# Optimization experiments

Measured on AMD Instinct MI355X. Metric: run time of the kernel, lower is better.

The kernel has to match this reference:

```python
import jax, jax.numpy as jnp
import numpy as np

RULE_START = 85
N_RULE = 20
N_OUTPUT = 33
N_RNN = 1024
T, B = 256, 256
ALPHA = 0.2
SIGMA = 0.05


def setup_inputs() -> dict:
    key = jax.random.key(0)
    ks = jax.random.split(key, 9)
    x = jax.random.normal(ks[0], (T, B, RULE_START + N_RULE), dtype=jnp.float32)
    # torch.rand_like -> uniform [0,1), scaled by sigma_rec (precomputed for all steps)
    noise = jax.random.uniform(ks[1], (T, B, N_RNN), dtype=jnp.float32) * SIGMA
    s = 0.05  # small init scale to keep softplus in a sane range
    W_sens = jax.random.normal(ks[2], (N_RNN, RULE_START), dtype=jnp.float32) * s
    b_sens = jax.random.normal(ks[3], (N_RNN,), dtype=jnp.float32) * s
    W_rule = jax.random.normal(ks[4], (N_RNN, N_RULE), dtype=jnp.float32) * s
    W_rec = jax.random.normal(ks[5], (N_RNN, N_RNN), dtype=jnp.float32) * s
    b_rec = jax.random.normal(ks[6], (N_RNN,), dtype=jnp.float32) * s
    W_out = jax.random.normal(ks[7], (N_OUTPUT, N_RNN), dtype=jnp.float32) * s
    b_out = jax.random.normal(ks[8], (N_OUTPUT,), dtype=jnp.float32) * s
    return {"x": x, "noise": noise, "W_sens": W_sens, "b_sens": b_sens,
            "W_rule": W_rule, "W_rec": W_rec, "b_rec": b_rec,
            "W_out": W_out, "b_out": b_out}


def reference(x, noise, W_sens, b_sens, W_rule, W_rec, b_rec, W_out, b_out):
    # x: [T, B, rule_start + n_rule]
    sensory = x[:, :, :RULE_START]
    rule = x[:, :, RULE_START:]
    # input projections applied once for all timesteps: [T, B, H]
    rnn_inputs = (jnp.einsum('tbi,hi->tbh', sensory, W_sens) + b_sens
                  + jnp.einsum('tbr,hr->tbh', rule, W_rule))

    h0 = jnp.zeros_like(rnn_inputs[0])  # [B, H]

    def step(h, inp_nz):
        inp, nz = inp_nz
        out = jax.nn.softplus(inp + nz + h @ W_rec.T + b_rec)
        h = ALPHA * out + (1.0 - ALPHA) * h
        return h, h

    _, hidden_states = jax.lax.scan(step, h0, (rnn_inputs, noise))  # [T, B, H]
    return jnp.einsum('tbh,oh->tbo', hidden_states, W_out) + b_out
```

## Files before the change

### kernel.cpp

```cpp
#include <hip/hip_runtime.h>
#include <cstdint>
#include <cstddef>

#define TSTEPS 256
#define NB     256
#define NH     1024
#define NIN    105
#define NOUT   33

using half8 = __attribute__((ext_vector_type(8))) _Float16;
using f32x4 = __attribute__((ext_vector_type(4))) float;


__global__ __launch_bounds__(256) void k_convert(
    const float* __restrict__ W_sens, const float* __restrict__ W_rule,
    const float* __restrict__ W_rec,  const float* __restrict__ W_out,
    _Float16* __restrict__ Wrecf, _Float16* __restrict__ Wcf,
    _Float16* __restrict__ Wof)
{
    int tid  = blockIdx.x * 256 + threadIdx.x;
    int lane = tid & 63;
    int orow = lane & 15;
    int col0 = (lane >> 4) * 8;
    if (tid < 64 * 32 * 64) {
        int kk = (tid >> 6) & 31, n = tid >> 11;
        int o = n * 16 + orow, k0 = kk * 32 + col0;
        const float* s = W_rec + (size_t)o * NH + k0;
        _Float16* d = Wrecf + (size_t)tid * 8;
        #pragma unroll
        for (int j = 0; j < 8; ++j) d[j] = (_Float16)s[j];
    } else if (tid < 64 * 32 * 64 + 64 * 4 * 64) {
        int t2 = tid - 64 * 32 * 64;
        int kk = (t2 >> 6) & 3, n = t2 >> 8;
        int o = n * 16 + orow, k0 = kk * 32 + col0;
        _Float16* d = Wcf + (size_t)t2 * 8;
        #pragma unroll
        for (int j = 0; j < 8; ++j) {
            int k = k0 + j;
            float v = 0.f;
            if (k < 85)       v = W_sens[o * 85 + k];
            else if (k < NIN) v = W_rule[o * 20 + (k - 85)];
            d[j] = (_Float16)v;
        }
    } else {
        int t3 = tid - (64 * 32 * 64 + 64 * 4 * 64);
        int kk = (t3 >> 6) & 31, n = t3 >> 11;
        int o = n * 16 + orow, k0 = kk * 32 + col0;
        _Float16* d = Wof + (size_t)t3 * 8;
        #pragma unroll
        for (int j = 0; j < 8; ++j)
            d[j] = (o < NOUT) ? (_Float16)W_out[(size_t)o * NH + k0 + j]
                              : (_Float16)0.f;
    }
}

__global__ __launch_bounds__(256) void k_init(int* __restrict__ flags)
{
    if (threadIdx.x < 256) flags[threadIdx.x] = 0;
}

__device__ __forceinline__ void in_gemm(
    const float* __restrict__ x, int tstep, int g, int m, int mrow, int q,
    const half8 wcb[4][4], const float nzf[4][4], const float bias[4],
    f32x4 pA[4])
{
    const float* xrow = x + ((size_t)tstep * NB + g * 32 + m * 16 + mrow) * NIN;
    half8 af[4];
    #pragma unroll
    for (int kk = 0; kk < 4; ++kk) {
        #pragma unroll
        for (int j = 0; j < 8; ++j) {
            int c = kk * 32 + q * 8 + j;
            float v = (c < NIN) ? xrow[c] : 0.f;
            af[kk][j] = (_Float16)v;
        }
    }
    #pragma unroll
    for (int nt = 0; nt < 4; ++nt) {
        f32x4 c = { nzf[nt][0] + bias[nt], nzf[nt][1] + bias[nt],
                    nzf[nt][2] + bias[nt], nzf[nt][3] + bias[nt] };
        #pragma unroll
        for (int kk = 0; kk < 4; ++kk)
            c = __builtin_amdgcn_mfma_f32_16x16x32_f16(af[kk], wcb[nt][kk], c,
                                                       0, 0, 0);
        pA[nt] = c;
    }
}

__global__ __launch_bounds__(512, 1) void k_rnn(
    const float* __restrict__ x, float* __restrict__ noise,
    const float* __restrict__ b_sens, const float* __restrict__ b_rec,
    const _Float16* __restrict__ Wrecf, const _Float16* __restrict__ Wcf,
    int* __restrict__ arr, int* __restrict__ xcdArr)
{
    __shared__ _Float16 Wl[4 * 32 * 64 * 8];
    __shared__ float red[3][8][64][4];
    __shared__ int sFast;

    const int tid  = threadIdx.x;
    const int blk  = blockIdx.x;
    const int g    = blk & 7, s = blk >> 3;
    const int wave = tid >> 6, lane = tid & 63;
    const int m    = wave & 1, kq = wave >> 1;
    const int mrow = lane & 15, q = lane >> 4;
    const half8* Wc8 = (const half8*)Wcf;
    _Float16* hist = (_Float16*)noise;
    volatile int* varr = (volatile int*)arr;

    {
        const float4* src = (const float4*)(Wrecf + (size_t)(4 * s) * (32 * 64 * 8));
        float4* dst = (float4*)Wl;
        for (int i = tid; i < 8192; i += 512) dst[i] = src[i];
    }

    int xcd;
    asm volatile("s_getreg_b32 %0, hwreg(20, 0, 4)" : "=s"(xcd));
    if (tid == 0)
        __hip_atomic_store(&xcdArr[blk], xcd + 1, __ATOMIC_RELEASE,
                           __HIP_MEMORY_SCOPE_AGENT);
    if (wave == 0) {
        int idx = g + (lane & 15) * 8;
        int v = 0;
        for (int it = 0; it < (1 << 22); ++it) {
            v = __hip_atomic_load(&xcdArr[idx], __ATOMIC_ACQUIRE,
                                  __HIP_MEMORY_SCOPE_AGENT);
            if (__all(v >= 1)) break;
            __builtin_amdgcn_s_sleep(8);
        }
        if (lane == 0) sFast = __all(v == xcd + 1) ? 1 : 0;
    }
    __syncthreads();
    const bool fast = (sFast != 0);

    float hm[4][4];
    f32x4 pA[4];
    float nzf[4][4];
    float bias[4];
    half8 wcb[4][4];
    #pragma unroll
    for (int nt = 0; nt < 4; ++nt)
        #pragma unroll
        for (int r = 0; r < 4; ++r) hm[nt][r] = 0.f;

    if (kq == 0) {
        #pragma unroll
        for (int nt = 0; nt < 4; ++nt) {
            int o = s * 64 + nt * 16 + mrow;
            bias[nt] = b_sens[o] + b_rec[o];
            #pragma unroll
            for (int kk = 0; kk < 4; ++kk)
                wcb[nt][kk] = Wc8[((4 * s + nt) * 4 + kk) * 64 + lane];
            #pragma unroll
            for (int r = 0; r < 4; ++r)
                nzf[nt][r] = noise[(size_t)(g * 32 + m * 16 + q * 4 + r) * NH
                                   + s * 64 + nt * 16 + mrow];
        }
    }
    __syncthreads();
    if (tid == 0) {
        if (fast) varr[g * 16 + s] = 1;
        else __hip_atomic_store(&arr[g * 16 + s], 1, __ATOMIC_RELAXED,
                                __HIP_MEMORY_SCOPE_AGENT);
    }
    if (kq == 0)
        in_gemm(x, 0, g, m, mrow, q, wcb, nzf, bias, pA);

    for (int t = 0; t < TSTEPS; ++t) {
        if (kq == 0 && t + 1 < TSTEPS) {
            #pragma unroll
            for (int nt = 0; nt < 4; ++nt)
                #pragma unroll
                for (int r = 0; r < 4; ++r)
                    nzf[nt][r] = noise[((size_t)(t + 1) * NB + g * 32 + m * 16
                                        + q * 4 + r) * NH
                                       + s * 64 + nt * 16 + mrow];
        }
        if (wave == 0) {
            int idx = g * 16 + (lane & 15);
            if (fast) {
                for (int it = 0; it < (1 << 22); ++it) {
                    asm volatile("buffer_inv sc0" ::: "memory");
                    int v = varr[idx];
                    if (__all(v >= t + 1)) break;
                    __builtin_amdgcn_s_sleep(1);
                }
            } else {
                for (int it = 0; it < (1 << 22); ++it) {
                    int v = __hip_atomic_load(&arr[idx], __ATOMIC_RELAXED,
                                              __HIP_MEMORY_SCOPE_AGENT);
                    if (__all(v >= t + 1)) break;
                    __builtin_amdgcn_s_sleep(1);
                }
            }
        }
        asm volatile("s_barrier" ::: "memory");
        if (!fast) __builtin_amdgcn_fence(__ATOMIC_ACQUIRE, "agent");

        f32x4 acc[4];
        #pragma unroll
        for (int nt = 0; nt < 4; ++nt) acc[nt] = (f32x4){0.f, 0.f, 0.f, 0.f};
        if (t > 0) {
            const _Float16* hR = hist + (size_t)(t - 1) * 524288
                                      + (size_t)g * 65536
                                      + (size_t)(m * 16 + mrow) * 1024
                                      + kq * 256 + q * 8;
            #pragma unroll
            for (int kkl = 0; kkl < 8; ++kkl) {
                half8 a = *(const half8*)(hR + kkl * 32);
                #pragma unroll
                for (int nt = 0; nt < 4; ++nt) {
                    half8 b = *(const half8*)&Wl[((nt * 32 + kq * 8 + kkl) * 64
                                                  + lane) * 8];
                    acc[nt] = __builtin_amdgcn_mfma_f32_16x16x32_f16(a, b,
                                                                acc[nt], 0, 0, 0);
                }
            }
        }
        if (kq != 0) {
            #pragma unroll
            for (int nt = 0; nt < 4; ++nt)
                *(f32x4*)&red[kq - 1][m * 4 + nt][lane][0] = acc[nt];
        }
        asm volatile("s_waitcnt lgkmcnt(0)\n\ts_barrier" ::: "memory");

        if (kq == 0) {
            const size_t hb = (size_t)t * 524288 + (size_t)g * 65536;
            #pragma unroll
            for (int nt = 0; nt < 4; ++nt) {
                f32x4 r0 = *(const f32x4*)&red[0][m * 4 + nt][lane][0];
                f32x4 r1 = *(const f32x4*)&red[1][m * 4 + nt][lane][0];
                f32x4 r2 = *(const f32x4*)&red[2][m * 4 + nt][lane][0];
                #pragma unroll
                for (int r = 0; r < 4; ++r) {
                    float v  = acc[nt][r] + r0[r] + r1[r] + r2[r] + pA[nt][r];
                    float sp = fmaxf(v, 0.f) + __logf(1.f + __expf(-fabsf(v)));
                    float hn = 0.2f * sp + 0.8f * hm[nt][r];
                    hm[nt][r] = hn;
                    hist[hb + (size_t)(m * 16 + q * 4 + r) * 1024
                            + s * 64 + nt * 16 + mrow] = (_Float16)hn;
                }
            }
        }
        asm volatile("s_waitcnt vmcnt(0) lgkmcnt(0)\n\ts_barrier" ::: "memory");
        if (tid == 0) {
            if (fast) varr[g * 16 + s] = t + 2;
            else {
                __builtin_amdgcn_fence(__ATOMIC_RELEASE, "agent");
                __hip_atomic_store(&arr[g * 16 + s], t + 2, __ATOMIC_RELAXED,
                                   __HIP_MEMORY_SCOPE_AGENT);
            }
        }
        if (kq == 0 && t + 1 < TSTEPS)
            in_gemm(x, t + 1, g, m, mrow, q, wcb, nzf, bias, pA);
    }
}

__global__ __launch_bounds__(256) void k_out(
    const _Float16* __restrict__ h16, const _Float16* __restrict__ Wof,
    const float* __restrict__ b_out, float* __restrict__ y)
{
    int blk  = blockIdx.x;
    int wave = threadIdx.x >> 6, lane = threadIdx.x & 63;
    int mrow = lane & 15, q = lane >> 4;
    int t  = blk >> 2;
    int b  = (blk & 3) * 64 + wave * 16 + mrow;
    size_t hb = (size_t)t * 524288 + (size_t)(b >> 5) * 65536
              + (size_t)(b & 31) * 1024;
    const half8* Wo8 = (const half8*)Wof;

    f32x4 acc[3];
    #pragma unroll
    for (int nt = 0; nt < 3; ++nt) acc[nt] = (f32x4){0.f, 0.f, 0.f, 0.f};

    #pragma unroll 4
    for (int kk = 0; kk < 32; ++kk) {
        half8 a = *(const half8*)(h16 + hb + kk * 32 + q * 8);
        #pragma unroll
        for (int nt = 0; nt < 3; ++nt) {
            half8 bb = Wo8[(nt * 32 + kk) * 64 + lane];
            acc[nt] = __builtin_amdgcn_mfma_f32_16x16x32_f16(a, bb, acc[nt],
                                                             0, 0, 0);
        }
    }
    #pragma unroll
    for (int nt = 0; nt < 3; ++nt) {
        int o = nt * 16 + mrow;
        if (o < NOUT) {
            float bo = b_out[o];
            #pragma unroll
            for (int r = 0; r < 4; ++r) {
                size_t R = (size_t)blk * 64 + wave * 16 + q * 4 + r;
                y[R * NOUT + o] = acc[nt][r] + bo;
            }
        }
    }
}

extern "C" void kernel_launch(void* const* d_in, const int* in_sizes, int n_in,
                              void* d_out, int out_size, void* d_ws, size_t ws_size,
                              hipStream_t stream) {
    const float* x      = (const float*)d_in[0];
    float*       noise  = (float*)d_in[1];
    const float* W_sens = (const float*)d_in[2];
    const float* b_sens = (const float*)d_in[3];
    const float* W_rule = (const float*)d_in[4];
    const float* W_rec  = (const float*)d_in[5];
    const float* b_rec  = (const float*)d_in[6];
    const float* W_out  = (const float*)d_in[7];
    const float* b_out  = (const float*)d_in[8];
    float*       y      = (float*)d_out;

    _Float16* wsp   = (_Float16*)d_ws;
    _Float16* Wrecf = wsp;
    _Float16* Wcf   = Wrecf + 1048576;
    _Float16* Wof   = Wcf   + 131072;
    int*      arr   = (int*)(Wof + 49152);
    int*      xcdArr= arr + 128;

    k_convert<<<dim3(600), dim3(256), 0, stream>>>(W_sens, W_rule, W_rec, W_out,
                                                   Wrecf, Wcf, Wof);
    k_init<<<dim3(1), dim3(256), 0, stream>>>(arr);
    k_rnn<<<dim3(128), dim3(512), 0, stream>>>(x, noise, b_sens, b_rec,
                                               Wrecf, Wcf, arr, xcdArr);
    k_out<<<dim3(1024), dim3(256), 0, stream>>>((const _Float16*)noise, Wof,
                                                b_out, y);
}
```

Baseline: 1.698 ms.

## Keep W_rec slice in registers and offload input projection to a dedicated wave

The recurrent kernel moves from 8 waves with W_rec staged in LDS to 6 waves. Four compute waves each hold their K-slice of W_rec in registers and process both 16-row M tiles. A fifth wave computes the next step's input projection plus noise into a double-buffered LDS array, and a sixth wave polls the inter-block flags. The cross-wave reduction now spreads the softplus/update work over all four compute waves instead of one K-quarter. The aim is to take the input GEMM off the serial critical path and remove LDS reads of the weights, at the cost of much higher register pressure (32 half8 weight registers per lane).

```diff
diff --git a/kernel.cpp b/kernel.cpp
--- a/kernel.cpp
+++ b/kernel.cpp
@@ -59,59 +59,25 @@
     if (threadIdx.x < 256) flags[threadIdx.x] = 0;
 }
 
-__device__ __forceinline__ void in_gemm(
-    const float* __restrict__ x, int tstep, int g, int m, int mrow, int q,
-    const half8 wcb[4][4], const float nzf[4][4], const float bias[4],
-    f32x4 pA[4])
-{
-    const float* xrow = x + ((size_t)tstep * NB + g * 32 + m * 16 + mrow) * NIN;
-    half8 af[4];
-    #pragma unroll
-    for (int kk = 0; kk < 4; ++kk) {
-        #pragma unroll
-        for (int j = 0; j < 8; ++j) {
-            int c = kk * 32 + q * 8 + j;
-            float v = (c < NIN) ? xrow[c] : 0.f;
-            af[kk][j] = (_Float16)v;
-        }
-    }
-    #pragma unroll
-    for (int nt = 0; nt < 4; ++nt) {
-        f32x4 c = { nzf[nt][0] + bias[nt], nzf[nt][1] + bias[nt],
-                    nzf[nt][2] + bias[nt], nzf[nt][3] + bias[nt] };
-        #pragma unroll
-        for (int kk = 0; kk < 4; ++kk)
-            c = __builtin_amdgcn_mfma_f32_16x16x32_f16(af[kk], wcb[nt][kk], c,
-                                                       0, 0, 0);
-        pA[nt] = c;
-    }
-}
-
-__global__ __launch_bounds__(512, 1) void k_rnn(
+__global__ __launch_bounds__(384, 2) void k_rnn(
     const float* __restrict__ x, float* __restrict__ noise,
     const float* __restrict__ b_sens, const float* __restrict__ b_rec,
     const _Float16* __restrict__ Wrecf, const _Float16* __restrict__ Wcf,
     int* __restrict__ arr, int* __restrict__ xcdArr)
 {
-    __shared__ _Float16 Wl[4 * 32 * 64 * 8];
-    __shared__ float red[3][8][64][4];
+    __shared__ float red[4][2][3][64][4];
+    __shared__ float pAl[2][2][4][64][4];
     __shared__ int sFast;
 
     const int tid  = threadIdx.x;
     const int blk  = blockIdx.x;
     const int g    = blk & 7, s = blk >> 3;
     const int wave = tid >> 6, lane = tid & 63;
-    const int m    = wave & 1, kq = wave >> 1;
     const int mrow = lane & 15, q = lane >> 4;
+    const half8* Wr8 = (const half8*)Wrecf;
     const half8* Wc8 = (const half8*)Wcf;
     _Float16* hist = (_Float16*)noise;
     volatile int* varr = (volatile int*)arr;
-
-    {
-        const float4* src = (const float4*)(Wrecf + (size_t)(4 * s) * (32 * 64 * 8));
-        float4* dst = (float4*)Wl;
-        for (int i = tid; i < 8192; i += 512) dst[i] = src[i];
-    }
 
     int xcd;
     asm volatile("s_getreg_b32 %0, hwreg(20, 0, 4)" : "=s"(xcd));
@@ -129,53 +95,91 @@
         }
         if (lane == 0) sFast = __all(v == xcd + 1) ? 1 : 0;
     }
+
+    half8 bf[4][8];
+    float hm[2][4];
+    half8 wcb[4][4];
+    float bias4[4];
+
+    if (wave < 4) {
+        #pragma unroll
+        for (int nt = 0; nt < 4; ++nt)
+            #pragma unroll
+            for (int kkl = 0; kkl < 8; ++kkl)
+                bf[nt][kkl] =
+                    Wr8[(size_t)((4 * s + nt) * 32 + wave * 8 + kkl) * 64 + lane];
+        #pragma unroll
+        for (int m = 0; m < 2; ++m)
+            #pragma unroll
+            for (int r = 0; r < 4; ++r) hm[m][r] = 0.f;
+    } else if (wave == 4) {
+        #pragma unroll
+        for (int nt = 0; nt < 4; ++nt) {
+            int o = s * 64 + nt * 16 + mrow;
+            bias4[nt] = b_sens[o] + b_rec[o];
+            #pragma unroll
+            for (int kk = 0; kk < 4; ++kk)
+                wcb[nt][kk] = Wc8[((4 * s + nt) * 4 + kk) * 64 + lane];
+        }
+        #pragma unroll
+        for (int m = 0; m < 2; ++m) {
+            const float* xrow = x + (size_t)(g * 32 + m * 16 + mrow) * NIN;
+            half8 af[4];
+            #pragma unroll
+            for (int kk = 0; kk < 4; ++kk)
+                #pragma unroll
+                for (int j = 0; j < 8; ++j) {
+                    int c = kk * 32 + q * 8 + j;
+                    af[kk][j] = (_Float16)((c < NIN) ? xrow[c] : 0.f);
+                }
+            #pragma unroll
+            for (int nt = 0; nt < 4; ++nt) {
+                f32x4 c;
+                #pragma unroll
+                for (int r = 0; r < 4; ++r)
+                    c[r] = noise[(size_t)(g * 32 + m * 16 + q * 4 + r) * NH
+                                 + s * 64 + nt * 16 + mrow] + bias4[nt];
+                #pragma unroll
+                for (int kk = 0; kk < 4; ++kk)
+                    c = __builtin_amdgcn_mfma_f32_16x16x32_f16(af[kk],
+                                                        wcb[nt][kk], c, 0, 0, 0);
+                *(f32x4*)&pAl[0][m][nt][lane][0] = c;
+            }
+        }
+    }
     __syncthreads();
     const bool fast = (sFast != 0);
-
-    float hm[4][4];
-    f32x4 pA[4];
-    float nzf[4][4];
-    float bias[4];
-    half8 wcb[4][4];
-    #pragma unroll
-    for (int nt = 0; nt < 4; ++nt)
-        #pragma unroll
-        for (int r = 0; r < 4; ++r) hm[nt][r] = 0.f;
-
-    if (kq == 0) {
-        #pragma unroll
-        for (int nt = 0; nt < 4; ++nt) {
-            int o = s * 64 + nt * 16 + mrow;
-            bias[nt] = b_sens[o] + b_rec[o];
-            #pragma unroll
-            for (int kk = 0; kk < 4; ++kk)
-                wcb[nt][kk] = Wc8[((4 * s + nt) * 4 + kk) * 64 + lane];
-            #pragma unroll
-            for (int r = 0; r < 4; ++r)
-                nzf[nt][r] = noise[(size_t)(g * 32 + m * 16 + q * 4 + r) * NH
-                                   + s * 64 + nt * 16 + mrow];
-        }
-    }
-    __syncthreads();
     if (tid == 0) {
         if (fast) varr[g * 16 + s] = 1;
         else __hip_atomic_store(&arr[g * 16 + s], 1, __ATOMIC_RELAXED,
                                 __HIP_MEMORY_SCOPE_AGENT);
     }
-    if (kq == 0)
-        in_gemm(x, 0, g, m, mrow, q, wcb, nzf, bias, pA);
 
     for (int t = 0; t < TSTEPS; ++t) {
-        if (kq == 0 && t + 1 < TSTEPS) {
-            #pragma unroll
-            for (int nt = 0; nt < 4; ++nt)
-                #pragma unroll
-                for (int r = 0; r < 4; ++r)
-                    nzf[nt][r] = noise[((size_t)(t + 1) * NB + g * 32 + m * 16
-                                        + q * 4 + r) * NH
-                                       + s * 64 + nt * 16 + mrow];
-        }
-        if (wave == 0) {
+        float xf[2][4][8];
+        float nzv[2][4][4];
+        if (wave == 4 && t + 1 < TSTEPS) {
+            #pragma unroll
+            for (int m = 0; m < 2; ++m) {
+                const float* xrow = x + ((size_t)(t + 1) * NB + g * 32 + m * 16
+                                         + mrow) * NIN;
+                #pragma unroll
+                for (int kk = 0; kk < 4; ++kk)
+                    #pragma unroll
+                    for (int j = 0; j < 8; ++j) {
+                        int c = kk * 32 + q * 8 + j;
+                        xf[m][kk][j] = (c < NIN) ? xrow[c] : 0.f;
+                    }
+                #pragma unroll
+                for (int nt = 0; nt < 4; ++nt)
+                    #pragma unroll
+                    for (int r = 0; r < 4; ++r)
+                        nzv[m][nt][r] =
+                            noise[((size_t)(t + 1) * NB + g * 32 + m * 16
+                                   + q * 4 + r) * NH + s * 64 + nt * 16 + mrow];
+            }
+        }
+        if (wave == 5) {
             int idx = g * 16 + (lane & 15);
             if (fast) {
                 for (int it = 0; it < (1 << 22); ++it) {
@@ -196,48 +200,88 @@
         asm volatile("s_barrier" ::: "memory");
         if (!fast) __builtin_amdgcn_fence(__ATOMIC_ACQUIRE, "agent");
 
-        f32x4 acc[4];
-        #pragma unroll
-        for (int nt = 0; nt < 4; ++nt) acc[nt] = (f32x4){0.f, 0.f, 0.f, 0.f};
-        if (t > 0) {
+        f32x4 acc[2][4];
+        #pragma unroll
+        for (int m = 0; m < 2; ++m)
+            #pragma unroll
+            for (int nt = 0; nt < 4; ++nt) acc[m][nt] = (f32x4){0.f,0.f,0.f,0.f};
+        if (wave < 4 && t > 0) {
             const _Float16* hR = hist + (size_t)(t - 1) * 524288
-                                      + (size_t)g * 65536
-                                      + (size_t)(m * 16 + mrow) * 1024
-                                      + kq * 256 + q * 8;
+                                      + (size_t)g * 65536 + wave * 256 + q * 8;
             #pragma unroll
             for (int kkl = 0; kkl < 8; ++kkl) {
-                half8 a = *(const half8*)(hR + kkl * 32);
+                half8 a0 = *(const half8*)(hR + (size_t)mrow * 1024 + kkl * 32);
+                half8 a1 = *(const half8*)(hR + (size_t)(16 + mrow) * 1024
+                                              + kkl * 32);
                 #pragma unroll
                 for (int nt = 0; nt < 4; ++nt) {
-                    half8 b = *(const half8*)&Wl[((nt * 32 + kq * 8 + kkl) * 64
-                                                  + lane) * 8];
-                    acc[nt] = __builtin_amdgcn_mfma_f32_16x16x32_f16(a, b,
-                                                                acc[nt], 0, 0, 0);
-                }
-            }
-        }
-        if (kq != 0) {
-            #pragma unroll
-            for (int nt = 0; nt < 4; ++nt)
-                *(f32x4*)&red[kq - 1][m * 4 + nt][lane][0] = acc[nt];
+                    acc[0][nt] = __builtin_amdgcn_mfma_f32_16x16x32_f16(
+                                     a0, bf[nt][kkl], acc[0][nt], 0, 0, 0);
+                    acc[1][nt] = __builtin_amdgcn_mfma_f32_16x16x32_f16(
+                                     a1, bf[nt][kkl], acc[1][nt], 0, 0, 0);
+                }
+            }
+        }
+        if (wave == 4 && t + 1 < TSTEPS) {
+            const int buf = (t + 1) & 1;
+            #pragma unroll
+            for (int m = 0; m < 2; ++m) {
+                half8 af[4];
+                #pragma unroll
+                for (int kk = 0; kk < 4; ++kk)
+                    #pragma unroll
+                    for (int j = 0; j < 8; ++j)
+                        af[kk][j] = (_Float16)xf[m][kk][j];
+                #pragma unroll
+                for (int nt = 0; nt < 4; ++nt) {
+                    f32x4 c = { nzv[m][nt][0] + bias4[nt],
+                                nzv[m][nt][1] + bias4[nt],
+                                nzv[m][nt][2] + bias4[nt],
+                                nzv[m][nt][3] + bias4[nt] };
+                    #pragma unroll
+                    for (int kk = 0; kk < 4; ++kk)
+                        c = __builtin_amdgcn_mfma_f32_16x16x32_f16(
+                                af[kk], wcb[nt][kk], c, 0, 0, 0);
+                    *(f32x4*)&pAl[buf][m][nt][lane][0] = c;
+                }
+            }
+        }
+        if (wave < 4) {
+            #pragma unroll
+            for (int m = 0; m < 2; ++m)
+                #pragma unroll
+                for (int nt = 0; nt < 4; ++nt)
+                    if (nt != wave) {
+                        int slot = (wave < nt) ? wave : wave - 1;
+                        *(f32x4*)&red[nt][m][slot][lane][0] = acc[m][nt];
+                    }
         }
         asm volatile("s_waitcnt lgkmcnt(0)\n\ts_barrier" ::: "memory");
 
-        if (kq == 0) {
+        if (wave < 4) {
+            f32x4 own[2];
+            #pragma unroll
+            for (int m = 0; m < 2; ++m) {
+                own[m] = acc[m][0];
+                #pragma unroll
+                for (int nt = 1; nt < 4; ++nt)
+                    if (wave == nt) own[m] = acc[m][nt];
+            }
             const size_t hb = (size_t)t * 524288 + (size_t)g * 65536;
             #pragma unroll
-            for (int nt = 0; nt < 4; ++nt) {
-                f32x4 r0 = *(const f32x4*)&red[0][m * 4 + nt][lane][0];
-                f32x4 r1 = *(const f32x4*)&red[1][m * 4 + nt][lane][0];
-                f32x4 r2 = *(const f32x4*)&red[2][m * 4 + nt][lane][0];
+            for (int m = 0; m < 2; ++m) {
+                f32x4 r0 = *(const f32x4*)&red[wave][m][0][lane][0];
+                f32x4 r1 = *(const f32x4*)&red[wave][m][1][lane][0];
+                f32x4 r2 = *(const f32x4*)&red[wave][m][2][lane][0];
+                f32x4 pa = *(const f32x4*)&pAl[t & 1][m][wave][lane][0];
                 #pragma unroll
                 for (int r = 0; r < 4; ++r) {
-                    float v  = acc[nt][r] + r0[r] + r1[r] + r2[r] + pA[nt][r];
+                    float v  = own[m][r] + r0[r] + r1[r] + r2[r] + pa[r];
                     float sp = fmaxf(v, 0.f) + __logf(1.f + __expf(-fabsf(v)));
-                    float hn = 0.2f * sp + 0.8f * hm[nt][r];
-                    hm[nt][r] = hn;
+                    float hn = 0.2f * sp + 0.8f * hm[m][r];
+                    hm[m][r] = hn;
                     hist[hb + (size_t)(m * 16 + q * 4 + r) * 1024
-                            + s * 64 + nt * 16 + mrow] = (_Float16)hn;
+                            + s * 64 + wave * 16 + mrow] = (_Float16)hn;
                 }
             }
         }
@@ -250,8 +294,6 @@
                                    __HIP_MEMORY_SCOPE_AGENT);
             }
         }
-        if (kq == 0 && t + 1 < TSTEPS)
-            in_gemm(x, t + 1, g, m, mrow, q, wcb, nzf, bias, pA);
     }
 }
 
@@ -320,7 +362,7 @@
     k_convert<<<dim3(600), dim3(256), 0, stream>>>(W_sens, W_rule, W_rec, W_out,
                                                    Wrecf, Wcf, Wof);
     k_init<<<dim3(1), dim3(256), 0, stream>>>(arr);
-    k_rnn<<<dim3(128), dim3(512), 0, stream>>>(x, noise, b_sens, b_rec,
+    k_rnn<<<dim3(128), dim3(384), 0, stream>>>(x, noise, b_sens, b_rec,
                                                Wrecf, Wcf, arr, xcdArr);
     k_out<<<dim3(1024), dim3(256), 0, stream>>>((const _Float16*)noise, Wof,
                                                 b_out, y);
```

Measured after the change: 2.654 ms. +56.3%, slower.
